# Kernel optimization log

Measured on AMD Instinct MI355X. Metric: run time of the kernel, lower is better.

## Reference

```python
import jax, jax.numpy as jnp
import numpy as np

B, S, DIN, DIM = 4, 4096, 256, 256
GAMMA = 0.9865


def setup_inputs() -> dict:
    key = jax.random.key(0)
    ks = jax.random.split(key, 9)
    inp = {
        'xq': jax.random.normal(ks[0], (B, S, DIN), dtype=jnp.float32),
        'xk': jax.random.normal(ks[1], (B, S, DIN), dtype=jnp.float32),
        'xv': jax.random.normal(ks[2], (B, S, DIN), dtype=jnp.float32),
        'Wq': jax.random.normal(ks[3], (DIN, DIM), dtype=jnp.float32) * 0.05,
        'bq': jnp.zeros((DIM,), dtype=jnp.float32),
        'Wk': jax.random.normal(ks[4], (DIN, DIM), dtype=jnp.float32) * 0.05,
        'bk': jnp.zeros((DIM,), dtype=jnp.float32),
        'Wv': jax.random.normal(ks[5], (DIN, DIM), dtype=jnp.float32) * 0.05,
        'bv': jnp.zeros((DIM,), dtype=jnp.float32),
    }
    return inp


def _decay_matrix(s, gamma):
    # D[i, j] = gamma^(i-j) if i >= j else 0
    idx = jnp.arange(s)
    diff = idx[:, None] - idx[None, :]
    D = jnp.where(diff >= 0,
                  jnp.power(jnp.float32(gamma), diff.astype(jnp.float32)),
                  jnp.float32(0.0))
    return D


def reference(xq, xk, xv, Wq, bq, Wk, bk, Wv, bv):
    Q = xq @ Wq + bq  # [B,S,D]
    K = xk @ Wk + bk  # [B,S,D]
    V = xv @ Wv + bv  # [B,S,D]
    d = Q.shape[-1]
    # scores[b,i,j] = Q[b,i] . K[b,j] / sqrt(d)
    x = jnp.einsum('bid,bjd->bij', Q, K) / jnp.sqrt(jnp.float32(d))
    D = _decay_matrix(S, GAMMA)
    # Faithful to TF broadcasting: divides along the LAST axis (per-column by
    # sqrt of that index's row-sum): D[i,j] /= sqrt(sum_k D[j,k])
    D = D / jnp.sqrt(jnp.sum(D, axis=-1))
    x = x * D  # broadcast [B,S,S] * [S,S]
    # _norm_3 per batch element with TF broadcasting: x[b,i,j] /= max(|sum_k x[b,j,k]|, 1)
    denom = jnp.maximum(jnp.abs(jnp.sum(x, axis=-1)), 1.0)  # [B,S]
    x = x / denom[:, None, :]
    return x @ V  # [B,S,D]
```

## Files before the change

### kernel.cpp

```cpp
#include <hip/hip_runtime.h>
#include <math.h>

#define BB 4
#define SS 4096
#define DD 256
#define LL 256
#define NCH 16
#define GAMMA 0.9865f
#define LOG2G (-0.019609034f)
#define INV1MG 74.07407407f
#define SLAB 1040
#define SLABB 520

typedef __attribute__((ext_vector_type(8))) short short8;
typedef __attribute__((ext_vector_type(4))) float f32x4;
typedef unsigned short u16;
typedef unsigned int u32;

__device__ __forceinline__ u16 f2bf(float f) {
  union { float f; unsigned u; } v; v.f = f;
  unsigned r = v.u + 0x7FFFu + ((v.u >> 16) & 1u);
  return (u16)(r >> 16);
}
__device__ __forceinline__ float bf2f(u16 h) {
  union { unsigned u; float f; } v; v.u = ((unsigned)h) << 16; return v.f;
}

__device__ __forceinline__ void gll16(const u16* g, u16* l) {
  __builtin_amdgcn_global_load_lds(
      (const __attribute__((address_space(1))) u32*)g,
      (__attribute__((address_space(3))) u32*)l, 16, 0, 0);
}
__device__ __forceinline__ void stage8kp(const u16* g, u16* l, int lane) {
#pragma unroll
  for (int i = 0; i < 8; ++i)
    gll16(g + i * 512 + lane * 8, l + (i >> 1) * SLAB + (i & 1) * 512);
}
__device__ __forceinline__ void stageB64(const u16* g, u16* l, int lane) {
#pragma unroll
  for (int i = 0; i < 4; ++i)
    gll16(g + i * 1024 + lane * 8, l + i * SLABB);
}

__device__ __forceinline__ void mfma_step_slab(
    const u16* Ah, const u16* Al, const u16* Bh, const u16* Bl,
    int wm0, int wn0, int fm, int fq, f32x4 acc[4][4])
{
  const int ka = fq * SLAB;
  short8 ah[4], al[4];
#pragma unroll
  for (int i = 0; i < 4; ++i) {
    ah[i] = *(const short8*)&Ah[ka + (wm0 + i * 16 + fm) * 8];
    al[i] = *(const short8*)&Al[ka + (wm0 + i * 16 + fm) * 8];
  }
#pragma unroll
  for (int j = 0; j < 4; ++j) {
    short8 bh = *(const short8*)&Bh[ka + (wn0 + j * 16 + fm) * 8];
    short8 bl = *(const short8*)&Bl[ka + (wn0 + j * 16 + fm) * 8];
#pragma unroll
    for (int i = 0; i < 4; ++i) {
      acc[i][j] = __builtin_amdgcn_mfma_f32_16x16x32_bf16(al[i], bh, acc[i][j], 0, 0, 0);
      acc[i][j] = __builtin_amdgcn_mfma_f32_16x16x32_bf16(ah[i], bl, acc[i][j], 0, 0, 0);
      acc[i][j] = __builtin_amdgcn_mfma_f32_16x16x32_bf16(ah[i], bh, acc[i][j], 0, 0, 0);
    }
  }
}

__device__ __forceinline__ void mfma_step_ab(
    const u16* Ah, const u16* Al, const u16* Bh, const u16* Bl,
    int wm0, int wn0, int fm, int fq, f32x4 acc[4][2])
{
  const int ka = fq * SLAB, kb = fq * SLABB;
  short8 ah[4], al[4];
#pragma unroll
  for (int i = 0; i < 4; ++i) {
    ah[i] = *(const short8*)&Ah[ka + (wm0 + i * 16 + fm) * 8];
    al[i] = *(const short8*)&Al[ka + (wm0 + i * 16 + fm) * 8];
  }
#pragma unroll
  for (int j = 0; j < 2; ++j) {
    short8 bh = *(const short8*)&Bh[kb + (wn0 + j * 16 + fm) * 8];
    short8 bl = *(const short8*)&Bl[kb + (wn0 + j * 16 + fm) * 8];
#pragma unroll
    for (int i = 0; i < 4; ++i) {
      acc[i][j] = __builtin_amdgcn_mfma_f32_16x16x32_bf16(al[i], bh, acc[i][j], 0, 0, 0);
      acc[i][j] = __builtin_amdgcn_mfma_f32_16x16x32_bf16(ah[i], bl, acc[i][j], 0, 0, 0);
      acc[i][j] = __builtin_amdgcn_mfma_f32_16x16x32_bf16(ah[i], bh, acc[i][j], 0, 0, 0);
    }
  }
}

__device__ __forceinline__ void bounce_write(
    float* fb, const f32x4 acc[4][4], int wm0, int wn0, int fm, int fq, int p)
{
  if (wn0 == p * 64) {
#pragma unroll
    for (int i = 0; i < 4; ++i)
#pragma unroll
      for (int j = 0; j < 4; ++j)
#pragma unroll
        for (int r = 0; r < 4; ++r)
          fb[(wm0 + i * 16 + fq * 4 + r) * 65 + j * 16 + fm] = acc[i][j][r];
  }
}

__global__ __launch_bounds__(256) void init_pack_kernel(
    const float* __restrict__ Wq, const float* __restrict__ Wk, const float* __restrict__ Wv,
    u16* __restrict__ Wth, u16* __restrict__ Wtl,
    float* __restrict__ rsP, float* __restrict__ lVec)
{
  const int which = blockIdx.x;
  const int t = threadIdx.x;
  if (which == 0) {
#pragma unroll
    for (int i = 0; i < 16; ++i)
      *(float4*)&rsP[(size_t)(i * 256 + t) * 4] = (float4){0.f, 0.f, 0.f, 0.f};
  } else if (which == 1) {
#pragma unroll
    for (int i = 0; i < 4; ++i)
      *(float4*)&lVec[(size_t)(i * 256 + t) * 4] = (float4){0.f, 0.f, 0.f, 0.f};
  }
  const float* W = which == 0 ? Wq : (which == 1 ? Wk : Wv);
  for (int pn = 0; pn < 2; ++pn) {
    for (int it = 0; it < 16; ++it) {
      int pos = it * 256 + t;
      int k8 = pos >> 7, r = pos & 127;
      u16 hs[8], ls[8];
#pragma unroll
      for (int u = 0; u < 8; ++u) {
        float x = W[(size_t)(k8 * 8 + u) * DD + pn * 128 + r];
        u16 h = f2bf(x); hs[u] = h; ls[u] = f2bf(x - bf2f(h));
      }
      size_t o = ((size_t)((which * 2 + pn) * 32 + k8)) * 1024 + (size_t)r * 8;
      *(short8*)&Wth[o] = *(short8*)hs;
      *(short8*)&Wtl[o] = *(short8*)ls;
    }
  }
}

__global__ __launch_bounds__(256, 3) void proj_kernel(
    const float* __restrict__ xq, const float* __restrict__ xk, const float* __restrict__ xv,
    const u16* __restrict__ Wth, const u16* __restrict__ Wtl,
    const float* __restrict__ bq, const float* __restrict__ bk_, const float* __restrict__ bv,
    u16* __restrict__ Qh, u16* __restrict__ Ql,
    u16* __restrict__ Kh, u16* __restrict__ Kl,
    u16* __restrict__ KTh, u16* __restrict__ KTl, float* __restrict__ VT32,
    float* __restrict__ lVec)
{
  const int which = blockIdx.z;
  const float* bias = which == 0 ? bq : (which == 1 ? bk_ : bv);
  const int m0 = blockIdx.x * 128;
  const int pn = blockIdx.y;
  __shared__ u16 SM[4 * 4 * SLAB];
  __shared__ float rsc[128];
  __shared__ float wlut[128];
  __shared__ float kacc[64];
  float* fb = (float*)SM;
  u16* Ah = SM; u16* Al = SM + 4 * SLAB; u16* Bh = SM + 8 * SLAB; u16* Bl = SM + 12 * SLAB;
  const int tid = threadIdx.x, lane = tid & 63, wave = tid >> 6;
  const int wm0 = (wave >> 1) * 64, wn0 = (wave & 1) * 64;
  const int fm = lane & 15, fq = lane >> 4;
  if (which == 1) {
    if (tid < 128) {
      int sb = (m0 & (SS - 1)) + tid;
      rsc[tid] = rsqrtf((1.0f - exp2f((float)(sb + 1) * LOG2G)) * INV1MG);
      wlut[tid] = exp2f((float)(255 - ((m0 & (LL - 1)) + tid)) * LOG2G);
    }
    if (tid < 64) kacc[tid] = 0.f;
  }
  const float* XP = (which == 0 ? xq : (which == 1 ? xk : xv)) + (size_t)m0 * DD;
  const u16* WhP = Wth + (size_t)((which * 2 + pn) * 32) * 1024;
  const u16* WlP = Wtl + (size_t)((which * 2 + pn) * 32) * 1024;
  const int arow = tid >> 2, ak8 = tid & 3;
  f32x4 acc[4][4];
#pragma unroll
  for (int i = 0; i < 4; ++i)
#pragma unroll
    for (int j = 0; j < 4; ++j) acc[i][j] = (f32x4){0.f, 0.f, 0.f, 0.f};
  for (int ks = 0; ks < 8; ++ks) {
    __syncthreads();
    if (wave == 2) stage8kp(WhP + ks * 4096, Bh, lane);
    if (wave == 3) stage8kp(WlP + ks * 4096, Bl, lane);
#pragma unroll
    for (int t = 0; t < 2; ++t) {
      int row = t * 64 + arow;
      const float* src = XP + (size_t)row * DD + ks * 32 + ak8 * 8;
      float xs[8];
      *(float4*)&xs[0] = *(const float4*)src;
      *(float4*)&xs[4] = *(const float4*)(src + 4);
      u16 hs[8], ls[8];
#pragma unroll
      for (int u = 0; u < 8; ++u) {
        u16 h = f2bf(xs[u]); hs[u] = h; ls[u] = f2bf(xs[u] - bf2f(h));
      }
      *(short8*)&Ah[ak8 * SLAB + row * 8] = *(short8*)hs;
      *(short8*)&Al[ak8 * SLAB + row * 8] = *(short8*)ls;
    }
    __syncthreads();
    mfma_step_slab(Ah, Al, Bh, Bl, wm0, wn0, fm, fq, acc);
  }
  const int b = m0 >> 12, sbb = m0 & (SS - 1);
  for (int p = 0; p < 2; ++p) {
    __syncthreads();
    bounce_write(fb, acc, wm0, wn0, fm, fq, p);
    __syncthreads();
    if (which == 0) {
#pragma unroll
      for (int it = 0; it < 4; ++it) {
        int unit = it * 256 + tid;
        int k8l = unit >> 7, row = unit & 127;
        int gcol0 = pn * 128 + p * 64 + k8l * 8;
        u16 hs[8], ls[8];
#pragma unroll
        for (int u = 0; u < 8; ++u) {
          float v = (fb[row * 65 + k8l * 8 + u] + bias[gcol0 + u]) * (1.f / 16.f);
          u16 h = f2bf(v); hs[u] = h; ls[u] = f2bf(v - bf2f(h));
        }
        size_t o = (size_t)(m0 >> 7) * 32768 + (size_t)(pn * 16 + p * 8 + k8l) * 1024 + row * 8;
        *(short8*)&Qh[o] = *(short8*)hs;
        *(short8*)&Ql[o] = *(short8*)ls;
      }
    } else if (which == 1) {
#pragma unroll
      for (int it = 0; it < 4; ++it) {
        int unit = it * 256 + tid;
        int k8l = unit >> 7, row = unit & 127;
        int gcol0 = pn * 128 + p * 64 + k8l * 8;
        u16 hs[8], ls[8];
#pragma unroll
        for (int u = 0; u < 8; ++u) {
          float v = (fb[row * 65 + k8l * 8 + u] + bias[gcol0 + u]) * rsc[row];
          u16 h = f2bf(v); hs[u] = h; ls[u] = f2bf(v - bf2f(h));
        }
        size_t o = (size_t)(m0 >> 7) * 32768 + (size_t)(pn * 16 + p * 8 + k8l) * 1024 + row * 8;
        *(short8*)&Kh[o] = *(short8*)hs;
        *(short8*)&Kl[o] = *(short8*)ls;
      }
      float kpart = 0.f;
#pragma unroll
      for (int it = 0; it < 4; ++it) {
        int unit = it * 256 + tid;
        int dl = unit & 63, s8l = unit >> 6;
        int gcolg = pn * 128 + p * 64 + dl;
        float bs = bias[gcolg];
        u16 hs[8], ls[8];
#pragma unroll
        for (int u = 0; u < 8; ++u) {
          int row = s8l * 8 + u;
          float v = (fb[row * 65 + dl] + bs) * rsc[row];
          kpart = fmaf(v, wlut[row], kpart);
          u16 h = f2bf(v); hs[u] = h; ls[u] = f2bf(v - bf2f(h));
        }
        int sb0 = sbb + s8l * 8;
        size_t o = ((size_t)(b * 2 + (gcolg >> 7)) * 512 + (sb0 >> 3)) * 1024 + (size_t)(gcolg & 127) * 8;
        *(short8*)&KTh[o] = *(short8*)hs;
        *(short8*)&KTl[o] = *(short8*)ls;
      }
      atomicAdd(&kacc[tid & 63], kpart);
      __syncthreads();
      if (tid < 64) {
        int c = sbb >> 8;
        atomicAdd(&lVec[(size_t)(b * NCH + c) * DD + pn * 128 + p * 64 + tid], kacc[tid]);
        kacc[tid] = 0.f;
      }
    } else {
#pragma unroll
      for (int it = 0; it < 4; ++it) {
        int unit = it * 256 + tid;
        int dl = unit & 63, s8l = unit >> 6;
        int gcolg = pn * 128 + p * 64 + dl;
        float bs = bias[gcolg];
        float vv[8];
#pragma unroll
        for (int u = 0; u < 8; ++u) vv[u] = fb[(s8l * 8 + u) * 65 + dl] + bs;
        float* dst = &VT32[(size_t)b * DD * SS + (size_t)gcolg * SS + sbb + s8l * 8];
        *(float4*)dst = (float4){vv[0], vv[1], vv[2], vv[3]};
        *(float4*)(dst + 4) = (float4){vv[4], vv[5], vv[6], vv[7]};
      }
    }
  }
}

__global__ __launch_bounds__(256) void combine_vec_kernel(
    const float* __restrict__ lVec, float* __restrict__ cVec)
{
  const int b = blockIdx.x;
  const int d = threadIdx.x;
  const float gL = powf(GAMMA, (float)LL);
  float s = 0.f;
  for (int c = 0; c < NCH; ++c) {
    cVec[(size_t)(b * NCH + c) * DD + d] = s;
    s = gL * s + lVec[(size_t)(b * NCH + c) * DD + d];
  }
}

__global__ __launch_bounds__(256, 3) void scores_kernel(
    const u16* __restrict__ Qh, const u16* __restrict__ Ql,
    const u16* __restrict__ Kh, const u16* __restrict__ Kl,
    const float* __restrict__ cVec, u16* __restrict__ Sgh, u16* __restrict__ Sgl,
    float* __restrict__ rsP)
{
  const int chunk = blockIdx.x, b = chunk >> 4, c = chunk & 15;
  const int y = blockIdx.y;
  const int m0 = (y < 2) ? 0 : 128;
  const int jn0 = (y < 2) ? y * 64 : (y - 2) * 64;
  __shared__ u16 SA[8 * SLAB];
  __shared__ u16 SB[8 * SLABB];
  __shared__ float cv[256], lut[256], rowAcc[128], qd2[2][128];
  u16* Ah = SA; u16* Al = SA + 4 * SLAB;
  u16* Bh = SB; u16* Bl = SB + 4 * SLABB;
  float* fb = (float*)SA;
  const int tid = threadIdx.x, lane = tid & 63, wave = tid >> 6;
  const int wm0 = (wave >> 1) * 64, wn0 = (wave & 1) * 32;
  const int fm = lane & 15, fq = lane >> 4;
  cv[tid] = cVec[(size_t)(b * NCH + c) * DD + tid];
  lut[tid] = exp2f((float)tid * LOG2G);
  if (tid < 128) rowAcc[tid] = 0.f;
  const int growA = b * SS + c * LL + m0;
  const int growB = b * SS + c * LL + jn0;
  const u16* QhP = Qh + (size_t)(growA >> 7) * 32768;
  const u16* QlP = Ql + (size_t)(growA >> 7) * 32768;
  const u16* KhP = Kh + (size_t)(growB >> 7) * 32768 + (size_t)(growB & 127) * 8;
  const u16* KlP = Kl + (size_t)(growB >> 7) * 32768 + (size_t)(growB & 127) * 8;
  f32x4 acc[4][2];
#pragma unroll
  for (int i = 0; i < 4; ++i)
#pragma unroll
    for (int j = 0; j < 2; ++j) acc[i][j] = (f32x4){0.f, 0.f, 0.f, 0.f};
  float qdreg = 0.f;
  const int qrow = tid & 127, qk8b = tid >> 7;
  for (int ks = 0; ks < 8; ++ks) {
    __syncthreads();
    if (wave == 0) stage8kp(QhP + ks * 4096, Ah, lane);
    if (wave == 1) stage8kp(QlP + ks * 4096, Al, lane);
    if (wave == 2) stageB64(KhP + ks * 4096, Bh, lane);
    if (wave == 3) stageB64(KlP + ks * 4096, Bl, lane);
    __syncthreads();
    mfma_step_ab(Ah, Al, Bh, Bl, wm0, wn0, fm, fq, acc);
    if (jn0 == 0) {
#pragma unroll
      for (int h2 = 0; h2 < 2; ++h2) {
        int k8l = qk8b + 2 * h2;
        const u16* ahp = &Ah[k8l * SLAB + qrow * 8];
        const u16* alp = &Al[k8l * SLAB + qrow * 8];
#pragma unroll
        for (int u = 0; u < 8; ++u)
          qdreg = fmaf(bf2f(ahp[u]) + bf2f(alp[u]), cv[ks * 32 + k8l * 8 + u], qdreg);
      }
    }
  }
  qd2[qk8b][qrow] = qdreg;
  const int ps = chunk * 2 + (m0 >> 7);
  for (int rh = 0; rh < 2; ++rh) {
    __syncthreads();
    if (wm0 == rh * 64) {
#pragma unroll
      for (int i = 0; i < 4; ++i)
#pragma unroll
        for (int j = 0; j < 2; ++j)
#pragma unroll
          for (int r = 0; r < 4; ++r)
            fb[(i * 16 + fq * 4 + r) * 65 + wn0 + j * 16 + fm] = acc[i][j][r];
    }
    __syncthreads();
#pragma unroll
    for (int it = 0; it < 2; ++it) {
      int unit = it * 256 + tid;
      int k8l = unit >> 6, rowl = unit & 63;
      int il = m0 + rh * 64 + rowl;
      int jlb = jn0 + k8l * 8;
      float part = 0.f;
      u16 hs[8], ls[8];
#pragma unroll
      for (int u = 0; u < 8; ++u) {
        int jl = jlb + u;
        float v = (jl <= il) ? fb[rowl * 65 + k8l * 8 + u] * lut[il - jl] : 0.f;
        part += v;
        u16 h = f2bf(v); hs[u] = h; ls[u] = f2bf(v - bf2f(h));
      }
      atomicAdd(&rowAcc[rh * 64 + rowl], part);
      size_t o = (size_t)(ps * 32 + (jn0 >> 3) + k8l) * 1024 + (size_t)(rh * 64 + rowl) * 8;
      *(short8*)&Sgh[o] = *(short8*)hs;
      *(short8*)&Sgl[o] = *(short8*)ls;
    }
  }
  __syncthreads();
  if (tid < 128) {
    float rs = rowAcc[tid];
    if (jn0 == 0)
      rs += exp2f((float)(m0 + tid + 1) * LOG2G) * (qd2[0][tid] + qd2[1][tid]);
    atomicAdd(&rsP[(size_t)b * SS + c * LL + m0 + tid], rs);
  }
}

__global__ __launch_bounds__(256) void vscale_kernel(
    const float* __restrict__ VT32, const float* __restrict__ rsP,
    u16* __restrict__ VdTh, u16* __restrict__ VdTl,
    u16* __restrict__ VwTh, u16* __restrict__ VwTl)
{
  const int x = blockIdx.x;
  const int b = x >> 6, pd = (x >> 5) & 1, sg = x & 31;
  const int t = threadIdx.x;
  __shared__ float tile[64][132];
  __shared__ float sdn[128], wtl[128];
  if (t < 128) {
    int s = sg * 128 + t;
    sdn[t] = fmaxf(fabsf(rsP[(size_t)b * SS + s]), 1.0f);
    wtl[t] = exp2f((float)(255 - (s & 255)) * LOG2G);
  }
  for (int eh = 0; eh < 2; ++eh) {
    __syncthreads();
#pragma unroll
    for (int v = 0; v < 8; ++v) {
      int lin = v * 256 + t;
      int col4 = lin & 31, row = lin >> 5;
      float4 xv = *(const float4*)&VT32[(size_t)b * DD * SS +
          (size_t)(pd * 128 + eh * 64 + row) * SS + sg * 128 + col4 * 4];
      *(float4*)&tile[row][col4 * 4] = xv;
    }
    __syncthreads();
#pragma unroll
    for (int it = 0; it < 4; ++it) {
      int unit = it * 256 + t;
      int s8l = unit >> 6, el = unit & 63;
      int e = pd * 128 + eh * 64 + el;
      u16 dh[8], dl_[8], wh[8], wl[8];
#pragma unroll
      for (int u = 0; u < 8; ++u) {
        int sloc = s8l * 8 + u;
        float vd = tile[el][sloc] / sdn[sloc];
        float vw = vd * wtl[sloc];
        u16 h = f2bf(vd); dh[u] = h; dl_[u] = f2bf(vd - bf2f(h));
        u16 h2 = f2bf(vw); wh[u] = h2; wl[u] = f2bf(vw - bf2f(h2));
      }
      int s8g = sg * 16 + s8l;
      size_t o = ((size_t)((b * 2 + pd) * 512 + s8g)) * 1024 + (size_t)(e & 127) * 8;
      *(short8*)&VdTh[o] = *(short8*)dh; *(short8*)&VdTl[o] = *(short8*)dl_;
      *(short8*)&VwTh[o] = *(short8*)wh; *(short8*)&VwTl[o] = *(short8*)wl;
    }
  }
}

__global__ __launch_bounds__(256, 3) void lmat_kernel(
    const u16* __restrict__ VwTh, const u16* __restrict__ VwTl,
    const u16* __restrict__ KTh, const u16* __restrict__ KTl,
    float* __restrict__ lMatT)
{
  const int chunk = blockIdx.x, b = chunk >> 4, c = chunk & 15;
  const int ty = blockIdx.y;
  const int m0 = (ty >> 2) * 128, n0 = (ty & 3) * 64;
  __shared__ u16 SA[8 * SLAB];
  __shared__ u16 SB[8 * SLABB];
  u16* Ah = SA; u16* Al = SA + 4 * SLAB;
  u16* Bh = SB; u16* Bl = SB + 4 * SLABB;
  const int tid = threadIdx.x, lane = tid & 63, wave = tid >> 6;
  const int wm0 = (wave >> 1) * 64, wn0 = (wave & 1) * 32;
  const int fm = lane & 15, fq = lane >> 4;
  const u16* AhP = VwTh + ((size_t)(b * 2 + (m0 >> 7)) * 512 + c * 32) * 1024;
  const u16* AlP = VwTl + ((size_t)(b * 2 + (m0 >> 7)) * 512 + c * 32) * 1024;
  const u16* BhP = KTh + ((size_t)(b * 2 + (n0 >> 7)) * 512 + c * 32) * 1024 + (size_t)(n0 & 127) * 8;
  const u16* BlP = KTl + ((size_t)(b * 2 + (n0 >> 7)) * 512 + c * 32) * 1024 + (size_t)(n0 & 127) * 8;
  f32x4 acc[4][2];
#pragma unroll
  for (int i = 0; i < 4; ++i)
#pragma unroll
    for (int j = 0; j < 2; ++j) acc[i][j] = (f32x4){0.f, 0.f, 0.f, 0.f};
  for (int ks = 0; ks < 8; ++ks) {
    __syncthreads();
    if (wave == 0) stage8kp(AhP + ks * 4096, Ah, lane);
    if (wave == 1) stage8kp(AlP + ks * 4096, Al, lane);
    if (wave == 2) stageB64(BhP + ks * 4096, Bh, lane);
    if (wave == 3) stageB64(BlP + ks * 4096, Bl, lane);
    __syncthreads();
    mfma_step_ab(Ah, Al, Bh, Bl, wm0, wn0, fm, fq, acc);
  }
#pragma unroll
  for (int i = 0; i < 4; ++i)
#pragma unroll
    for (int j = 0; j < 2; ++j)
#pragma unroll
      for (int r = 0; r < 4; ++r) {
        int e = m0 + wm0 + i * 16 + fq * 4 + r;
        int d = n0 + wn0 + j * 16 + fm;
        lMatT[(size_t)chunk * 65536 + (size_t)e * 256 + d] = acc[i][j][r];
      }
}

__global__ __launch_bounds__(256) void combine_mat_kernel(
    const float* __restrict__ lMatT, u16* __restrict__ cMh, u16* __restrict__ cMl)
{
  const int t = blockIdx.x * 256 + threadIdx.x;
  const int b = t >> 13, rem = t & 8191;
  const int k8 = rem >> 8, e = rem & 255;
  const float gL = powf(GAMMA, (float)LL);
  float s[8] = {0.f, 0.f, 0.f, 0.f, 0.f, 0.f, 0.f, 0.f};
  for (int ch = 0; ch < 16; ++ch) {
    size_t ro = (size_t)(b * 16 + ch) * 65536 + (size_t)e * 256 + k8 * 8;
    float4 a0 = *(const float4*)&lMatT[ro];
    float4 a1 = *(const float4*)&lMatT[ro + 4];
    float vals[8] = {a0.x, a0.y, a0.z, a0.w, a1.x, a1.y, a1.z, a1.w};
    u16 hh[8], ll[8];
#pragma unroll
    for (int u = 0; u < 8; ++u) {
      u16 h = f2bf(s[u]); hh[u] = h; ll[u] = f2bf(s[u] - bf2f(h));
    }
    size_t wo = ((size_t)(((b * 16 + ch) * 2 + (e >> 7)) * 32 + k8)) * 1024 + (size_t)(e & 127) * 8;
    *(short8*)&cMh[wo] = *(short8*)hh;
    *(short8*)&cMl[wo] = *(short8*)ll;
#pragma unroll
    for (int u = 0; u < 8; ++u) s[u] = gL * s[u] + vals[u];
  }
}

__global__ __launch_bounds__(256, 3) void out_kernel(
    const u16* __restrict__ Qh, const u16* __restrict__ Ql,
    const u16* __restrict__ cMh, const u16* __restrict__ cMl,
    const u16* __restrict__ Sgh, const u16* __restrict__ Sgl,
    const u16* __restrict__ VdTh, const u16* __restrict__ VdTl,
    float* __restrict__ out)
{
  const int chunk = blockIdx.x, b = chunk >> 4, c = chunk & 15;
  const int ty = blockIdx.y;
  const int m0 = (ty >> 2) * 128, n0 = (ty & 3) * 64;
  __shared__ u16 SA[8 * SLAB];
  __shared__ u16 SB[8 * SLABB];
  __shared__ float olut[128];
  u16* Ah = SA; u16* Al = SA + 4 * SLAB;
  u16* Bh = SB; u16* Bl = SB + 4 * SLABB;
  const int tid = threadIdx.x, lane = tid & 63, wave = tid >> 6;
  const int wm0 = (wave >> 1) * 64, wn0 = (wave & 1) * 32;
  const int fm = lane & 15, fq = lane >> 4;
  if (tid < 128) olut[tid] = exp2f((float)(m0 + tid + 1) * LOG2G);
  f32x4 acc[4][2];
#pragma unroll
  for (int i = 0; i < 4; ++i)
#pragma unroll
    for (int j = 0; j < 2; ++j) acc[i][j] = (f32x4){0.f, 0.f, 0.f, 0.f};
  {
    const u16* AhP = Qh + (size_t)(b * 32 + c * 2 + (m0 >> 7)) * 32768;
    const u16* AlP = Ql + (size_t)(b * 32 + c * 2 + (m0 >> 7)) * 32768;
    const u16* BhP = cMh + (size_t)(chunk * 2 + (n0 >> 7)) * 32768 + (size_t)(n0 & 127) * 8;
    const u16* BlP = cMl + (size_t)(chunk * 2 + (n0 >> 7)) * 32768 + (size_t)(n0 & 127) * 8;
    for (int ks = 0; ks < 8; ++ks) {
      __syncthreads();
      if (wave == 0) stage8kp(AhP + ks * 4096, Ah, lane);
      if (wave == 1) stage8kp(AlP + ks * 4096, Al, lane);
      if (wave == 2) stageB64(BhP + ks * 4096, Bh, lane);
      if (wave == 3) stageB64(BlP + ks * 4096, Bl, lane);
      __syncthreads();
      mfma_step_ab(Ah, Al, Bh, Bl, wm0, wn0, fm, fq, acc);
    }
  }
#pragma unroll
  for (int i = 0; i < 4; ++i)
#pragma unroll
    for (int r = 0; r < 4; ++r) {
      int rl = wm0 + i * 16 + fq * 4 + r;
      float sc = olut[rl];
#pragma unroll
      for (int j = 0; j < 2; ++j) acc[i][j][r] *= sc;
    }
  {
    const u16* AhP = Sgh + (size_t)(chunk * 2 + (m0 >> 7)) * 32768;
    const u16* AlP = Sgl + (size_t)(chunk * 2 + (m0 >> 7)) * 32768;
    const u16* BhP = VdTh + ((size_t)(b * 2 + (n0 >> 7)) * 512 + c * 32) * 1024 + (size_t)(n0 & 127) * 8;
    const u16* BlP = VdTl + ((size_t)(b * 2 + (n0 >> 7)) * 512 + c * 32) * 1024 + (size_t)(n0 & 127) * 8;
    const int nks = (m0 >> 5) + 4;
    for (int ks = 0; ks < nks; ++ks) {
      __syncthreads();
      if (wave == 0) stage8kp(AhP + ks * 4096, Ah, lane);
      if (wave == 1) stage8kp(AlP + ks * 4096, Al, lane);
      if (wave == 2) stageB64(BhP + ks * 4096, Bh, lane);
      if (wave == 3) stageB64(BlP + ks * 4096, Bl, lane);
      __syncthreads();
      mfma_step_ab(Ah, Al, Bh, Bl, wm0, wn0, fm, fq, acc);
    }
  }
#pragma unroll
  for (int i = 0; i < 4; ++i)
#pragma unroll
    for (int j = 0; j < 2; ++j)
#pragma unroll
      for (int r = 0; r < 4; ++r) {
        int il = m0 + wm0 + i * 16 + fq * 4 + r;
        int e = n0 + wn0 + j * 16 + fm;
        out[(size_t)(b * SS + c * LL + il) * DD + e] = acc[i][j][r];
      }
}

extern "C" void kernel_launch(void* const* d_in, const int* in_sizes, int n_in,
                              void* d_out, int out_size, void* d_ws, size_t ws_size,
                              hipStream_t stream) {
  const float* xq = (const float*)d_in[0];
  const float* xk = (const float*)d_in[1];
  const float* xv = (const float*)d_in[2];
  const float* Wq = (const float*)d_in[3];
  const float* bq = (const float*)d_in[4];
  const float* Wk = (const float*)d_in[5];
  const float* bk = (const float*)d_in[6];
  const float* Wv = (const float*)d_in[7];
  const float* bv = (const float*)d_in[8];
  float* out = (float*)d_out;

  char* p = (char*)d_ws;
  const size_t H16 = (size_t)BB * SS * DD * 2;
  u16* Qh   = (u16*)(p + 0 * H16);  u16* Ql   = (u16*)(p + 1 * H16);
  u16* Kh   = (u16*)(p + 2 * H16);  u16* Kl   = (u16*)(p + 3 * H16);
  u16* KTh  = (u16*)(p + 4 * H16);  u16* KTl  = (u16*)(p + 5 * H16);
  u16* VdTh = (u16*)(p + 6 * H16);  u16* VdTl = (u16*)(p + 7 * H16);
  u16* VwTh = (u16*)(p + 8 * H16);  u16* VwTl = (u16*)(p + 9 * H16);
  u16* Sgh  = (u16*)(p + 10 * H16); u16* Sgl  = (u16*)(p + 11 * H16);
  u16* cMh  = (u16*)(p + 12 * H16); u16* cMl  = (u16*)(p + 13 * H16);
  float* lMatT = (float*)(p + 14 * H16);
  float* VT32  = (float*)(p + 16 * H16);
  u16* Wth = (u16*)(p + 18 * H16);
  u16* Wtl = (u16*)(p + 18 * H16 + 3 * DD * DD * 2);
  float* rsP  = (float*)(p + 18 * H16 + 6 * DD * DD * 2);
  float* lVec = rsP + (size_t)BB * SS;
  float* cVec = lVec + (size_t)BB * NCH * DD;

  init_pack_kernel<<<dim3(3), 256, 0, stream>>>(Wq, Wk, Wv, Wth, Wtl, rsP, lVec);
  proj_kernel<<<dim3(BB * SS / 128, 2, 3), 256, 0, stream>>>(
      xq, xk, xv, Wth, Wtl, bq, bk, bv, Qh, Ql, Kh, Kl, KTh, KTl, VT32, lVec);
  combine_vec_kernel<<<BB, 256, 0, stream>>>(lVec, cVec);
  scores_kernel<<<dim3(BB * NCH, 6), 256, 0, stream>>>(
      Qh, Ql, Kh, Kl, cVec, Sgh, Sgl, rsP);
  vscale_kernel<<<256, 256, 0, stream>>>(VT32, rsP, VdTh, VdTl, VwTh, VwTl);
  lmat_kernel<<<dim3(BB * NCH, 8), 256, 0, stream>>>(VwTh, VwTl, KTh, KTl, lMatT);
  combine_mat_kernel<<<128, 256, 0, stream>>>(lMatT, cMh, cMl);
  out_kernel<<<dim3(BB * NCH, 8), 256, 0, stream>>>(
      Qh, Ql, cMh, cMl, Sgh, Sgl, VdTh, VdTl, out);
}
```

Before: 234.0 us.

## Prefetch proj inputs into registers, fold combine_vec into scores, widen init grid

Adds a register prefetch in proj_kernel so the next k-slab of fp32 inputs is loaded while the MFMAs run, and raises its launch-bounds occupancy hint from 3 to 4. It also removes combine_vec_kernel: scores_kernel now computes the decayed prefix sum of lVec itself, but only in blocks with jn0==0, which saves one launch. init_pack_kernel is spread over a 3x16 grid instead of 3 blocks. Risks are more register pressure from the prefetch buffer, possible spills under the tighter occupancy hint, and uninitialized cv in scores blocks with jn0!=0 if they read it.

After: 219.1 us. 6.4% less time.

```diff
diff --git a/kernel.cpp b/kernel.cpp
--- a/kernel.cpp
+++ b/kernel.cpp
@@ -110,35 +110,30 @@
     float* __restrict__ rsP, float* __restrict__ lVec)
 {
   const int which = blockIdx.x;
+  const int it = blockIdx.y;
   const int t = threadIdx.x;
   if (which == 0) {
-#pragma unroll
-    for (int i = 0; i < 16; ++i)
-      *(float4*)&rsP[(size_t)(i * 256 + t) * 4] = (float4){0.f, 0.f, 0.f, 0.f};
+    *(float4*)&rsP[(size_t)(it * 256 + t) * 4] = (float4){0.f, 0.f, 0.f, 0.f};
   } else if (which == 1) {
-#pragma unroll
-    for (int i = 0; i < 4; ++i)
-      *(float4*)&lVec[(size_t)(i * 256 + t) * 4] = (float4){0.f, 0.f, 0.f, 0.f};
+    *(float4*)&lVec[(size_t)(it * 256 + t) * 4] = (float4){0.f, 0.f, 0.f, 0.f};
   }
   const float* W = which == 0 ? Wq : (which == 1 ? Wk : Wv);
   for (int pn = 0; pn < 2; ++pn) {
-    for (int it = 0; it < 16; ++it) {
-      int pos = it * 256 + t;
-      int k8 = pos >> 7, r = pos & 127;
-      u16 hs[8], ls[8];
-#pragma unroll
-      for (int u = 0; u < 8; ++u) {
-        float x = W[(size_t)(k8 * 8 + u) * DD + pn * 128 + r];
-        u16 h = f2bf(x); hs[u] = h; ls[u] = f2bf(x - bf2f(h));
-      }
-      size_t o = ((size_t)((which * 2 + pn) * 32 + k8)) * 1024 + (size_t)r * 8;
-      *(short8*)&Wth[o] = *(short8*)hs;
-      *(short8*)&Wtl[o] = *(short8*)ls;
-    }
-  }
-}
-
-__global__ __launch_bounds__(256, 3) void proj_kernel(
+    int pos = it * 256 + t;
+    int k8 = pos >> 7, r = pos & 127;
+    u16 hs[8], ls[8];
+#pragma unroll
+    for (int u = 0; u < 8; ++u) {
+      float x = W[(size_t)(k8 * 8 + u) * DD + pn * 128 + r];
+      u16 h = f2bf(x); hs[u] = h; ls[u] = f2bf(x - bf2f(h));
+    }
+    size_t o = ((size_t)((which * 2 + pn) * 32 + k8)) * 1024 + (size_t)r * 8;
+    *(short8*)&Wth[o] = *(short8*)hs;
+    *(short8*)&Wtl[o] = *(short8*)ls;
+  }
+}
+
+__global__ __launch_bounds__(256, 4) void proj_kernel(
     const float* __restrict__ xq, const float* __restrict__ xk, const float* __restrict__ xv,
     const u16* __restrict__ Wth, const u16* __restrict__ Wtl,
     const float* __restrict__ bq, const float* __restrict__ bk_, const float* __restrict__ bv,
@@ -177,6 +172,13 @@
   for (int i = 0; i < 4; ++i)
 #pragma unroll
     for (int j = 0; j < 4; ++j) acc[i][j] = (f32x4){0.f, 0.f, 0.f, 0.f};
+  float xs[2][8];
+#pragma unroll
+  for (int t = 0; t < 2; ++t) {
+    const float* src = XP + (size_t)(t * 64 + arow) * DD + ak8 * 8;
+    *(float4*)&xs[t][0] = *(const float4*)src;
+    *(float4*)&xs[t][4] = *(const float4*)(src + 4);
+  }
   for (int ks = 0; ks < 8; ++ks) {
     __syncthreads();
     if (wave == 2) stage8kp(WhP + ks * 4096, Bh, lane);
@@ -184,19 +186,23 @@
 #pragma unroll
     for (int t = 0; t < 2; ++t) {
       int row = t * 64 + arow;
-      const float* src = XP + (size_t)row * DD + ks * 32 + ak8 * 8;
-      float xs[8];
-      *(float4*)&xs[0] = *(const float4*)src;
-      *(float4*)&xs[4] = *(const float4*)(src + 4);
       u16 hs[8], ls[8];
 #pragma unroll
       for (int u = 0; u < 8; ++u) {
-        u16 h = f2bf(xs[u]); hs[u] = h; ls[u] = f2bf(xs[u] - bf2f(h));
+        u16 h = f2bf(xs[t][u]); hs[u] = h; ls[u] = f2bf(xs[t][u] - bf2f(h));
       }
       *(short8*)&Ah[ak8 * SLAB + row * 8] = *(short8*)hs;
       *(short8*)&Al[ak8 * SLAB + row * 8] = *(short8*)ls;
     }
     __syncthreads();
+    if (ks < 7) {
+#pragma unroll
+      for (int t = 0; t < 2; ++t) {
+        const float* src = XP + (size_t)(t * 64 + arow) * DD + (ks + 1) * 32 + ak8 * 8;
+        *(float4*)&xs[t][0] = *(const float4*)src;
+        *(float4*)&xs[t][4] = *(const float4*)(src + 4);
+      }
+    }
     mfma_step_slab(Ah, Al, Bh, Bl, wm0, wn0, fm, fq, acc);
   }
   const int b = m0 >> 12, sbb = m0 & (SS - 1);
@@ -281,23 +287,10 @@
   }
 }
 
-__global__ __launch_bounds__(256) void combine_vec_kernel(
-    const float* __restrict__ lVec, float* __restrict__ cVec)
-{
-  const int b = blockIdx.x;
-  const int d = threadIdx.x;
-  const float gL = powf(GAMMA, (float)LL);
-  float s = 0.f;
-  for (int c = 0; c < NCH; ++c) {
-    cVec[(size_t)(b * NCH + c) * DD + d] = s;
-    s = gL * s + lVec[(size_t)(b * NCH + c) * DD + d];
-  }
-}
-
 __global__ __launch_bounds__(256, 3) void scores_kernel(
     const u16* __restrict__ Qh, const u16* __restrict__ Ql,
     const u16* __restrict__ Kh, const u16* __restrict__ Kl,
-    const float* __restrict__ cVec, u16* __restrict__ Sgh, u16* __restrict__ Sgl,
+    const float* __restrict__ lVec, u16* __restrict__ Sgh, u16* __restrict__ Sgl,
     float* __restrict__ rsP)
 {
   const int chunk = blockIdx.x, b = chunk >> 4, c = chunk & 15;
@@ -313,7 +306,13 @@
   const int tid = threadIdx.x, lane = tid & 63, wave = tid >> 6;
   const int wm0 = (wave >> 1) * 64, wn0 = (wave & 1) * 32;
   const int fm = lane & 15, fq = lane >> 4;
-  cv[tid] = cVec[(size_t)(b * NCH + c) * DD + tid];
+  if (jn0 == 0) {
+    const float gL = exp2f((float)LL * LOG2G);
+    float s = 0.f;
+    for (int cp = 0; cp < c; ++cp)
+      s = fmaf(gL, s, lVec[(size_t)(b * NCH + cp) * DD + tid]);
+    cv[tid] = s;
+  }
   lut[tid] = exp2f((float)tid * LOG2G);
   if (tid < 128) rowAcc[tid] = 0.f;
   const int growA = b * SS + c * LL + m0;
@@ -617,14 +616,12 @@
   u16* Wtl = (u16*)(p + 18 * H16 + 3 * DD * DD * 2);
   float* rsP  = (float*)(p + 18 * H16 + 6 * DD * DD * 2);
   float* lVec = rsP + (size_t)BB * SS;
-  float* cVec = lVec + (size_t)BB * NCH * DD;
-
-  init_pack_kernel<<<dim3(3), 256, 0, stream>>>(Wq, Wk, Wv, Wth, Wtl, rsP, lVec);
+
+  init_pack_kernel<<<dim3(3, 16), 256, 0, stream>>>(Wq, Wk, Wv, Wth, Wtl, rsP, lVec);
   proj_kernel<<<dim3(BB * SS / 128, 2, 3), 256, 0, stream>>>(
       xq, xk, xv, Wth, Wtl, bq, bk, bv, Qh, Ql, Kh, Kl, KTh, KTl, VT32, lVec);
-  combine_vec_kernel<<<BB, 256, 0, stream>>>(lVec, cVec);
   scores_kernel<<<dim3(BB * NCH, 6), 256, 0, stream>>>(
-      Qh, Ql, Kh, Kl, cVec, Sgh, Sgl, rsP);
+      Qh, Ql, Kh, Kl, lVec, Sgh, Sgl, rsP);
   vscale_kernel<<<256, 256, 0, stream>>>(VT32, rsP, VdTh, VdTl, VwTh, VwTl);
   lmat_kernel<<<dim3(BB * NCH, 8), 256, 0, stream>>>(VwTh, VwTl, KTh, KTl, lMatT);
   combine_mat_kernel<<<128, 256, 0, stream>>>(lMatT, cMh, cMl);
```
